# Kernel tuning notes

Hardware: AMD Instinct MI355X
Metric: run time of the kernel (lower is better)

## Reference

```python
import jax, jax.numpy as jnp
import numpy as np

N_NODES = 50000
N_EDGES = 800000
IN_FEAT = 128
HEADS = 4
UNITS = 16
LEAKY_ALPHA = 0.2  # tf.nn.leaky_relu default


def setup_inputs() -> dict:
    key = jax.random.key(0)
    k1, k2, k3, k4, k5 = jax.random.split(key, 5)
    x = jax.random.normal(k1, (N_NODES, IN_FEAT), dtype=jnp.float32)
    edge_index = jax.random.randint(k2, (N_EDGES, 2), 0, N_NODES, dtype=jnp.int32)
    # Dense kernel (glorot-ish scaling), no bias (use_bias=False)
    W = jax.random.normal(k3, (IN_FEAT, HEADS * UNITS), dtype=jnp.float32) * (1.0 / np.sqrt(IN_FEAT))
    glorot = np.sqrt(2.0 / (1 + UNITS)).astype(np.float32)
    att_w1 = jax.random.normal(k4, (HEADS, 1, UNITS), dtype=jnp.float32) * glorot
    att_w2 = jax.random.normal(k5, (HEADS, 1, UNITS), dtype=jnp.float32) * glorot
    return {"x": x, "edge_index": edge_index, "W": W, "att_w1": att_w1, "att_w2": att_w2}


def reference(x, edge_index, W, att_w1, att_w2):
    n_nodes = x.shape[0]
    h = x @ W  # [N, H*U]
    snd_idx = edge_index[:, 0]
    rcv_idx = edge_index[:, 1]
    # gather per-edge features, split into heads -> [H, E, U]
    sender = h[snd_idx].reshape(-1, HEADS, UNITS).transpose(1, 0, 2)
    receiver = h[rcv_idx].reshape(-1, HEADS, UNITS).transpose(1, 0, 2)
    # per-edge, per-head attention logits [H, E]
    att = jnp.sum(att_w1 * sender, axis=-1) + jnp.sum(att_w2 * receiver, axis=-1)
    att = jnp.where(att > 0, att, LEAKY_ALPHA * att)
    # segment softmax over receiver neighborhoods, per head
    seg_max = jax.vmap(lambda a: jax.ops.segment_max(a, rcv_idx, num_segments=n_nodes))(att)  # [H, N]
    e = jnp.exp(att - seg_max[:, rcv_idx])
    denom = jax.vmap(lambda a: jax.ops.segment_sum(a, rcv_idx, num_segments=n_nodes))(e)  # [H, N]
    alpha = e / denom[:, rcv_idx]  # [H, E]
    # weighted scatter-sum of sender features -> [H, N, U]
    out = jax.vmap(lambda v: jax.ops.segment_sum(v, rcv_idx, num_segments=n_nodes))(sender * alpha[:, :, None])
    # concat heads -> [N, H*U]; activation is None (identity)
    return out.transpose(1, 0, 2).reshape(n_nodes, HEADS * UNITS)
```

## Files before the change

### kernel.cpp

```cpp
#include <hip/hip_runtime.h>
#include <math.h>

#define N_NODES 50000
#define N_EDGES 800000
#define IN_FEAT 128
#define HEADS   4
#define UNITS   16
#define OUTF    64
#define LEAKY   0.2f

#define NB      196
#define BCAP    5120
#define GEMM_BLKS 782
#define A_BLOCKS  391
#define EPB     8

typedef __attribute__((ext_vector_type(8))) short bf16x8;
typedef __attribute__((ext_vector_type(4))) float f32x4;

__device__ __forceinline__ unsigned short f2bf(float f) {
    unsigned u = __float_as_uint(f);
    unsigned r = u + 0x7FFFu + ((u >> 16) & 1u);
    return (unsigned short)(r >> 16);
}

union SharedU {
    struct { unsigned short xl[64 * 136]; unsigned short wt[64 * 136]; } g;
    struct { int2 stage[2048]; int hist[256], s[256], excl[256],
             gbase[256], cur[256]; } a;
};

__global__ __launch_bounds__(256) void wt_prep(const float* __restrict__ W,
                                               unsigned short* __restrict__ Wt_g,
                                               int* __restrict__ bucket_cnt) {
    int idx = blockIdx.x * 256 + threadIdx.x;
    if (blockIdx.x == 0 && threadIdx.x < NB) bucket_cnt[threadIdx.x] = 0;
    if (idx < IN_FEAT * OUTF) {
        int k = idx >> 6, c = idx & 63;
        Wt_g[c * IN_FEAT + k] = f2bf(W[idx]);
    }
}

__global__ __launch_bounds__(256) void fused_gemm_bucketA(const float* __restrict__ x,
                                                          const unsigned short* __restrict__ Wt_g,
                                                          const float* __restrict__ w1,
                                                          const float* __restrict__ w2,
                                                          const int2* __restrict__ ei,
                                                          unsigned short* __restrict__ hg,
                                                          float* __restrict__ a1,
                                                          float* __restrict__ a2,
                                                          int* __restrict__ bucket_cnt,
                                                          int2* __restrict__ buckets) {
    __shared__ SharedU sh;
    const int t = threadIdx.x;

    if (blockIdx.x >= GEMM_BLKS) {
        const int e0 = (blockIdx.x - GEMM_BLKS) * 2048;
        sh.a.hist[t] = 0;
        __syncthreads();

        int2 ed[EPB]; int bk[EPB];
        #pragma unroll
        for (int j = 0; j < EPB; ++j) {
            int e = e0 + t + j * 256;
            if (e < N_EDGES) {
                ed[j] = ei[e];
                bk[j] = ed[j].y >> 8;
                atomicAdd(&sh.a.hist[bk[j]], 1);
            } else bk[j] = -1;
        }
        __syncthreads();
        int v = sh.a.hist[t];
        sh.a.s[t] = v;
        __syncthreads();
        #pragma unroll
        for (int off = 1; off < 256; off <<= 1) {
            int u = (t >= off) ? sh.a.s[t - off] : 0;
            __syncthreads();
            sh.a.s[t] += u;
            __syncthreads();
        }
        sh.a.excl[t] = sh.a.s[t] - v;
        sh.a.cur[t] = 0;
        if (t < NB) sh.a.gbase[t] = atomicAdd(&bucket_cnt[t], v);
        __syncthreads();
        #pragma unroll
        for (int j = 0; j < EPB; ++j) {
            if (bk[j] >= 0) {
                int p = sh.a.excl[bk[j]] + atomicAdd(&sh.a.cur[bk[j]], 1);
                sh.a.stage[p] = ed[j];
            }
        }
        __syncthreads();
        const int total = min(2048, N_EDGES - e0);
        for (int i = t; i < total; i += 256) {
            int2 vv = sh.a.stage[i];
            int b = vv.y >> 8;
            buckets[(size_t)b * BCAP + sh.a.gbase[b] + (i - sh.a.excl[b])] = vv;
        }
        return;
    }

    const int node0 = blockIdx.x * 64;
    unsigned short* xl = sh.g.xl;
    unsigned short* wt = sh.g.wt;

    #pragma unroll
    for (int it = 0; it < 8; ++it) {
        int idx = t + 256 * it;
        int r = idx >> 5, q = idx & 31;
        int node = node0 + r;
        float4 v = make_float4(0.f, 0.f, 0.f, 0.f);
        if (node < N_NODES) v = *(const float4*)(x + (size_t)node * IN_FEAT + q * 4);
        ushort4 b;
        b.x = f2bf(v.x); b.y = f2bf(v.y); b.z = f2bf(v.z); b.w = f2bf(v.w);
        *(ushort4*)&xl[r * 136 + q * 4] = b;
    }
    {
        const ushort4* Wt4 = (const ushort4*)Wt_g;
        #pragma unroll
        for (int it = 0; it < 8; ++it) {
            int idx = t + 256 * it;
            int c = idx >> 5, u = idx & 31;
            *(ushort4*)&wt[c * 136 + u * 4] = Wt4[idx];
        }
    }
    __syncthreads();

    const int lane = t & 63, wv = t >> 6;
    const int m = lane & 15, quad = lane >> 4;
    const int n0 = wv * 16;

    f32x4 acc[4] = {{0,0,0,0},{0,0,0,0},{0,0,0,0},{0,0,0,0}};
    #pragma unroll
    for (int kc = 0; kc < 4; ++kc) {
        bf16x8 af = *(bf16x8*)&xl[(n0 + m) * 136 + kc * 32 + quad * 8];
        #pragma unroll
        for (int ct = 0; ct < 4; ++ct) {
            bf16x8 bfr = *(bf16x8*)&wt[(ct * 16 + m) * 136 + kc * 32 + quad * 8];
            acc[ct] = __builtin_amdgcn_mfma_f32_16x16x32_bf16(af, bfr, acc[ct], 0, 0, 0);
        }
    }

    #pragma unroll
    for (int ct = 0; ct < 4; ++ct) {
        const float u1 = w1[ct * 16 + m];
        const float u2 = w2[ct * 16 + m];
        #pragma unroll
        for (int r = 0; r < 4; ++r) {
            float p1 = acc[ct][r] * u1;
            float p2 = acc[ct][r] * u2;
            p1 += __shfl_xor(p1, 1, 64); p1 += __shfl_xor(p1, 2, 64);
            p1 += __shfl_xor(p1, 4, 64); p1 += __shfl_xor(p1, 8, 64);
            p2 += __shfl_xor(p2, 1, 64); p2 += __shfl_xor(p2, 2, 64);
            p2 += __shfl_xor(p2, 4, 64); p2 += __shfl_xor(p2, 8, 64);
            if (m == 0) {
                int node = node0 + n0 + quad * 4 + r;
                if (node < N_NODES) {
                    a1[node * 4 + ct] = p1;
                    a2[node * 4 + ct] = p2;
                }
            }
        }
    }

    __syncthreads();
    unsigned short* hl = sh.g.xl;
    #pragma unroll
    for (int ct = 0; ct < 4; ++ct)
        #pragma unroll
        for (int r = 0; r < 4; ++r)
            hl[(n0 + quad * 4 + r) * 72 + ct * 16 + m] = f2bf(acc[ct][r]);
    __syncthreads();
    #pragma unroll
    for (int it = 0; it < 2; ++it) {
        int u = t + 256 * it;
        int r = u >> 3, cg = u & 7;
        int node = node0 + r;
        if (node < N_NODES)
            *(uint4*)&hg[(size_t)node * OUTF + cg * 8] = *(uint4*)&hl[r * 72 + cg * 8];
    }
}

__global__ __launch_bounds__(256) void bucketB(const int2* __restrict__ buckets,
                                               const int* __restrict__ bucket_cnt,
                                               int* __restrict__ edge_snd,
                                               int* __restrict__ rs,
                                               int* __restrict__ re) {
    __shared__ int hist[256], cur[256], s[256];
    __shared__ int snds[BCAP];
    const int b = blockIdx.x;
    const int t = threadIdx.x;
    const int cnt = bucket_cnt[b];
    hist[t] = 0;
    __syncthreads();
    for (int i = t; i < cnt; i += 256)
        atomicAdd(&hist[buckets[(size_t)b * BCAP + i].y & 255], 1);
    __syncthreads();
    int v = hist[t];
    s[t] = v;
    __syncthreads();
    #pragma unroll
    for (int off = 1; off < 256; off <<= 1) {
        int u = (t >= off) ? s[t - off] : 0;
        __syncthreads();
        s[t] += u;
        __syncthreads();
    }
    const int excl = s[t] - v;
    cur[t] = excl;
    const int node = b * 256 + t;
    if (node < N_NODES) {
        rs[node] = b * BCAP + excl;
        re[node] = b * BCAP + excl + v;
    }
    __syncthreads();
    for (int i = t; i < cnt; i += 256) {
        int2 vv = buckets[(size_t)b * BCAP + i];
        int p = atomicAdd(&cur[vv.y & 255], 1);
        snds[p] = vv.x;
    }
    __syncthreads();
    for (int i = t; i < cnt; i += 256) edge_snd[(size_t)b * BCAP + i] = snds[i];
}

__global__ __launch_bounds__(256, 8) void gather_kernel(const int* __restrict__ rs,
                                                        const int* __restrict__ re,
                                                        const int* __restrict__ edge_snd,
                                                        const float* __restrict__ a1,
                                                        const float* __restrict__ a2,
                                                        const unsigned short* __restrict__ h,
                                                        float* __restrict__ out) {
    const int wave = threadIdx.x >> 6;
    const int lane = threadIdx.x & 63;
    const int n = blockIdx.x * 4 + wave;
    if (n >= N_NODES) return;
    const int sub  = lane >> 3;
    const int li   = lane & 7;
    const int head = li >> 1;
    const int base = rs[n];
    const int end  = re[n];
    if (end <= base) {
        if (sub == 0) {
            *(float4*)(out + (size_t)n * OUTF + li * 8)     = make_float4(0.f, 0.f, 0.f, 0.f);
            *(float4*)(out + (size_t)n * OUTF + li * 8 + 4) = make_float4(0.f, 0.f, 0.f, 0.f);
        }
        return;
    }
    const float a2h = a2[n * 4 + head];
    const uint4* h4 = (const uint4*)h;

    float acc[8] = {0.f,0.f,0.f,0.f,0.f,0.f,0.f,0.f};
    float den = 0.f;

    for (int i = base; i < end; i += 16) {
        #pragma unroll
        for (int g = 0; g < 2; ++g) {
            int eraw = i + g * 8 + sub;
            int eidx = min(eraw, end - 1);
            int s = edge_snd[eidx];
            float t0 = a1[s * 4 + head] + a2h;
            t0 = t0 > 0.f ? t0 : LEAKY * t0;
            float e = (eraw < end) ? __expf(t0) : 0.f;
            uint4 hv = h4[(unsigned)(s * 8 + li)];
            const unsigned hw[4] = {hv.x, hv.y, hv.z, hv.w};
            #pragma unroll
            for (int q = 0; q < 4; ++q) {
                acc[q*2+0] = fmaf(e, __uint_as_float(hw[q] << 16),         acc[q*2+0]);
                acc[q*2+1] = fmaf(e, __uint_as_float(hw[q] & 0xFFFF0000u), acc[q*2+1]);
            }
            den += e;
        }
    }

    #pragma unroll
    for (int off = 8; off <= 32; off <<= 1) {
        #pragma unroll
        for (int q = 0; q < 8; ++q) acc[q] += __shfl_xor(acc[q], off, 64);
        den += __shfl_xor(den, off, 64);
    }

    if (sub == 0) {
        float inv = 1.f / den;
        *(float4*)(out + (size_t)n * OUTF + li * 8) =
            make_float4(acc[0] * inv, acc[1] * inv, acc[2] * inv, acc[3] * inv);
        *(float4*)(out + (size_t)n * OUTF + li * 8 + 4) =
            make_float4(acc[4] * inv, acc[5] * inv, acc[6] * inv, acc[7] * inv);
    }
}

extern "C" void kernel_launch(void* const* d_in, const int* in_sizes, int n_in,
                              void* d_out, int out_size, void* d_ws, size_t ws_size,
                              hipStream_t stream) {
    const float* x  = (const float*)d_in[0];
    const int2*  ei = (const int2*)d_in[1];
    const float* W  = (const float*)d_in[2];
    const float* w1 = (const float*)d_in[3];
    const float* w2 = (const float*)d_in[4];
    float* out = (float*)d_out;

    unsigned short* h = (unsigned short*)d_ws;
    float* a1         = (float*)(h + (size_t)N_NODES * OUTF);
    float* a2         = a1 + (size_t)N_NODES * HEADS;
    int2*  buckets    = (int2*)(a2 + (size_t)N_NODES * HEADS);
    int*   edge_snd   = (int*)(buckets + (size_t)NB * BCAP);
    int*   rs         = edge_snd + (size_t)NB * BCAP;
    int*   re         = rs + N_NODES;
    int*   bucket_cnt = re + N_NODES;
    unsigned short* Wt_g = (unsigned short*)(bucket_cnt + NB);

    wt_prep<<<32, 256, 0, stream>>>(W, Wt_g, bucket_cnt);
    fused_gemm_bucketA<<<GEMM_BLKS + A_BLOCKS, 256, 0, stream>>>(x, Wt_g, w1, w2, ei,
                                                                 h, a1, a2,
                                                                 bucket_cnt, buckets);
    bucketB<<<NB, 256, 0, stream>>>(buckets, bucket_cnt, edge_snd, rs, re);
    gather_kernel<<<(N_NODES + 3) / 4, 256, 0, stream>>>(rs, re, edge_snd, a1, a2, h, out);
}
```

Measured before the change: 134.8 us.

## Precompute per-edge attention exponentials in bucketB and fold W transpose into GEMM

Removes the wt_prep kernel: every GEMM block now converts and transposes W from fp32 itself, and bucket_cnt is cleared with a memset. bucketB is widened to 1024 threads, stages the bucket in shared memory to avoid reading it twice, and computes all four heads' leaky-relu exponentials per edge, writing them to a new edge_e array. The gather kernel then reads the precomputed e values instead of doing a random a1 lookup and an exp. The cost is an extra 16 bytes per edge written and read, plus a scattered 2-byte shared-memory transpose store of W in every GEMM block.

```diff
diff --git a/kernel.cpp b/kernel.cpp
--- a/kernel.cpp
+++ b/kernel.cpp
@@ -30,19 +30,8 @@
              gbase[256], cur[256]; } a;
 };
 
-__global__ __launch_bounds__(256) void wt_prep(const float* __restrict__ W,
-                                               unsigned short* __restrict__ Wt_g,
-                                               int* __restrict__ bucket_cnt) {
-    int idx = blockIdx.x * 256 + threadIdx.x;
-    if (blockIdx.x == 0 && threadIdx.x < NB) bucket_cnt[threadIdx.x] = 0;
-    if (idx < IN_FEAT * OUTF) {
-        int k = idx >> 6, c = idx & 63;
-        Wt_g[c * IN_FEAT + k] = f2bf(W[idx]);
-    }
-}
-
 __global__ __launch_bounds__(256) void fused_gemm_bucketA(const float* __restrict__ x,
-                                                          const unsigned short* __restrict__ Wt_g,
+                                                          const float* __restrict__ W,
                                                           const float* __restrict__ w1,
                                                           const float* __restrict__ w2,
                                                           const int2* __restrict__ ei,
@@ -117,12 +106,17 @@
         *(ushort4*)&xl[r * 136 + q * 4] = b;
     }
     {
-        const ushort4* Wt4 = (const ushort4*)Wt_g;
+        const float4* W4 = (const float4*)W;
         #pragma unroll
         for (int it = 0; it < 8; ++it) {
-            int idx = t + 256 * it;
-            int c = idx >> 5, u = idx & 31;
-            *(ushort4*)&wt[c * 136 + u * 4] = Wt4[idx];
+            int idx4 = t + 256 * it;
+            float4 v = W4[idx4];
+            int flat = idx4 * 4;
+            int k = flat >> 6, c = flat & 63;
+            wt[(c + 0) * 136 + k] = f2bf(v.x);
+            wt[(c + 1) * 136 + k] = f2bf(v.y);
+            wt[(c + 2) * 136 + k] = f2bf(v.z);
+            wt[(c + 3) * 136 + k] = f2bf(v.w);
         }
     }
     __syncthreads();
@@ -182,53 +176,67 @@
     }
 }
 
-__global__ __launch_bounds__(256) void bucketB(const int2* __restrict__ buckets,
-                                               const int* __restrict__ bucket_cnt,
-                                               int* __restrict__ edge_snd,
-                                               int* __restrict__ rs,
-                                               int* __restrict__ re) {
+__global__ __launch_bounds__(1024) void bucketB(const int2* __restrict__ buckets,
+                                                const int* __restrict__ bucket_cnt,
+                                                const float* __restrict__ a1,
+                                                const float* __restrict__ a2,
+                                                int* __restrict__ edge_snd,
+                                                float* __restrict__ edge_e,
+                                                int* __restrict__ rs,
+                                                int* __restrict__ re) {
     __shared__ int hist[256], cur[256], s[256];
-    __shared__ int snds[BCAP];
+    __shared__ int2 stage[BCAP];
     const int b = blockIdx.x;
     const int t = threadIdx.x;
     const int cnt = bucket_cnt[b];
-    hist[t] = 0;
-    __syncthreads();
-    for (int i = t; i < cnt; i += 256)
-        atomicAdd(&hist[buckets[(size_t)b * BCAP + i].y & 255], 1);
-    __syncthreads();
-    int v = hist[t];
-    s[t] = v;
+    if (t < 256) hist[t] = 0;
+    __syncthreads();
+    for (int i = t; i < cnt; i += 1024) {
+        int2 vv = buckets[(size_t)b * BCAP + i];
+        stage[i] = vv;
+        atomicAdd(&hist[vv.y & 255], 1);
+    }
+    __syncthreads();
+    if (t < 256) s[t] = hist[t];
     __syncthreads();
     #pragma unroll
     for (int off = 1; off < 256; off <<= 1) {
-        int u = (t >= off) ? s[t - off] : 0;
-        __syncthreads();
-        s[t] += u;
-        __syncthreads();
-    }
-    const int excl = s[t] - v;
-    cur[t] = excl;
-    const int node = b * 256 + t;
-    if (node < N_NODES) {
-        rs[node] = b * BCAP + excl;
-        re[node] = b * BCAP + excl + v;
-    }
-    __syncthreads();
-    for (int i = t; i < cnt; i += 256) {
-        int2 vv = buckets[(size_t)b * BCAP + i];
+        int u = (t < 256 && t >= off) ? s[t - off] : 0;
+        __syncthreads();
+        if (t < 256) s[t] += u;
+        __syncthreads();
+    }
+    if (t < 256) {
+        const int v = hist[t];
+        const int excl = s[t] - v;
+        cur[t] = excl;
+        const int node = b * 256 + t;
+        if (node < N_NODES) {
+            rs[node] = b * BCAP + excl;
+            re[node] = b * BCAP + excl + v;
+        }
+    }
+    __syncthreads();
+    for (int i = t; i < cnt; i += 1024) {
+        int2 vv = stage[i];
         int p = atomicAdd(&cur[vv.y & 255], 1);
-        snds[p] = vv.x;
-    }
-    __syncthreads();
-    for (int i = t; i < cnt; i += 256) edge_snd[(size_t)b * BCAP + i] = snds[i];
+        float4 s1 = *(const float4*)(a1 + (size_t)vv.x * 4);
+        float4 s2 = *(const float4*)(a2 + (size_t)vv.y * 4);
+        float t0 = s1.x + s2.x; t0 = t0 > 0.f ? t0 : LEAKY * t0;
+        float t1 = s1.y + s2.y; t1 = t1 > 0.f ? t1 : LEAKY * t1;
+        float t2 = s1.z + s2.z; t2 = t2 > 0.f ? t2 : LEAKY * t2;
+        float t3 = s1.w + s2.w; t3 = t3 > 0.f ? t3 : LEAKY * t3;
+        float4 e4 = make_float4(__expf(t0), __expf(t1), __expf(t2), __expf(t3));
+        size_t q = (size_t)b * BCAP + p;
+        edge_snd[q] = vv.x;
+        *(float4*)(edge_e + q * 4) = e4;
+    }
 }
 
 __global__ __launch_bounds__(256, 8) void gather_kernel(const int* __restrict__ rs,
                                                         const int* __restrict__ re,
                                                         const int* __restrict__ edge_snd,
-                                                        const float* __restrict__ a1,
-                                                        const float* __restrict__ a2,
+                                                        const float* __restrict__ edge_e,
                                                         const unsigned short* __restrict__ h,
                                                         float* __restrict__ out) {
     const int wave = threadIdx.x >> 6;
@@ -247,7 +255,6 @@
         }
         return;
     }
-    const float a2h = a2[n * 4 + head];
     const uint4* h4 = (const uint4*)h;
 
     float acc[8] = {0.f,0.f,0.f,0.f,0.f,0.f,0.f,0.f};
@@ -259,9 +266,8 @@
             int eraw = i + g * 8 + sub;
             int eidx = min(eraw, end - 1);
             int s = edge_snd[eidx];
-            float t0 = a1[s * 4 + head] + a2h;
-            t0 = t0 > 0.f ? t0 : LEAKY * t0;
-            float e = (eraw < end) ? __expf(t0) : 0.f;
+            float ev = edge_e[(size_t)eidx * 4 + head];
+            float e = (eraw < end) ? ev : 0.f;
             uint4 hv = h4[(unsigned)(s * 8 + li)];
             const unsigned hw[4] = {hv.x, hv.y, hv.z, hv.w};
             #pragma unroll
@@ -303,16 +309,17 @@
     float* a1         = (float*)(h + (size_t)N_NODES * OUTF);
     float* a2         = a1 + (size_t)N_NODES * HEADS;
     int2*  buckets    = (int2*)(a2 + (size_t)N_NODES * HEADS);
-    int*   edge_snd   = (int*)(buckets + (size_t)NB * BCAP);
+    float* edge_e     = (float*)(buckets + (size_t)NB * BCAP);
+    int*   edge_snd   = (int*)(edge_e + (size_t)NB * BCAP * 4);
     int*   rs         = edge_snd + (size_t)NB * BCAP;
     int*   re         = rs + N_NODES;
     int*   bucket_cnt = re + N_NODES;
-    unsigned short* Wt_g = (unsigned short*)(bucket_cnt + NB);
-
-    wt_prep<<<32, 256, 0, stream>>>(W, Wt_g, bucket_cnt);
-    fused_gemm_bucketA<<<GEMM_BLKS + A_BLOCKS, 256, 0, stream>>>(x, Wt_g, w1, w2, ei,
+
+    hipMemsetAsync(bucket_cnt, 0, NB * sizeof(int), stream);
+    fused_gemm_bucketA<<<GEMM_BLKS + A_BLOCKS, 256, 0, stream>>>(x, W, w1, w2, ei,
                                                                  h, a1, a2,
                                                                  bucket_cnt, buckets);
-    bucketB<<<NB, 256, 0, stream>>>(buckets, bucket_cnt, edge_snd, rs, re);
-    gather_kernel<<<(N_NODES + 3) / 4, 256, 0, stream>>>(rs, re, edge_snd, a1, a2, h, out);
-}
+    bucketB<<<NB, 1024, 0, stream>>>(buckets, bucket_cnt, a1, a2,
+                                     edge_snd, edge_e, rs, re);
+    gather_kernel<<<(N_NODES + 3) / 4, 256, 0, stream>>>(rs, re, edge_snd, edge_e, h, out);
+}
```

New measurement: 136.5 us. Within noise of the previous version (+1.3%).

## Fold attention vectors into weights, use wave-shuffle scans, widen bucketB blocks

Applied to the files above, without the earlier changes.

Precomputes W·att_w1 and W·att_w2 per head in the prep kernel, split into bf16 hi/lo parts, so the attention logits come from one extra MFMA per k-chunk instead of a shuffle-reduction epilogue. Replaces the shared-memory Hillis-Steele scans in both bucketing kernels with wave-level shuffle scans plus cross-wave offsets, and simplifies the global scatter offset. bucketB now runs 1024 threads, stages edges in LDS to avoid reading them twice, and writes sender ids directly to global, dropping the final copy loop. Extra LDS in the GEMM path and the launch_bounds occupancy hint may change occupancy, and the bf16 hi/lo split slightly changes logit precision.

```diff
diff --git a/kernel.cpp b/kernel.cpp
--- a/kernel.cpp
+++ b/kernel.cpp
@@ -23,36 +23,58 @@
     unsigned r = u + 0x7FFFu + ((u >> 16) & 1u);
     return (unsigned short)(r >> 16);
 }
+__device__ __forceinline__ float bf2f(unsigned short b) {
+    return __uint_as_float(((unsigned)b) << 16);
+}
 
 union SharedU {
-    struct { unsigned short xl[64 * 136]; unsigned short wt[64 * 136]; } g;
-    struct { int2 stage[2048]; int hist[256], s[256], excl[256],
-             gbase[256], cur[256]; } a;
+    struct { unsigned short xl[64 * 136]; unsigned short wt[64 * 136];
+             unsigned short wa[16 * 136]; } g;
+    struct { int2 stage[2048]; int hist[256], cur[256], adj[256], wsum[4]; } a;
 };
 
-__global__ __launch_bounds__(256) void wt_prep(const float* __restrict__ W,
-                                               unsigned short* __restrict__ Wt_g,
-                                               int* __restrict__ bucket_cnt) {
+__global__ __launch_bounds__(256) void prep(const float* __restrict__ W,
+                                            const float* __restrict__ w1,
+                                            const float* __restrict__ w2,
+                                            unsigned short* __restrict__ Wt_g,
+                                            unsigned short* __restrict__ Wea_g,
+                                            int* __restrict__ bucket_cnt) {
     int idx = blockIdx.x * 256 + threadIdx.x;
-    if (blockIdx.x == 0 && threadIdx.x < NB) bucket_cnt[threadIdx.x] = 0;
+    if (idx < NB) bucket_cnt[idx] = 0;
     if (idx < IN_FEAT * OUTF) {
         int k = idx >> 6, c = idx & 63;
         Wt_g[c * IN_FEAT + k] = f2bf(W[idx]);
     }
-}
-
-__global__ __launch_bounds__(256) void fused_gemm_bucketA(const float* __restrict__ x,
-                                                          const unsigned short* __restrict__ Wt_g,
-                                                          const float* __restrict__ w1,
-                                                          const float* __restrict__ w2,
-                                                          const int2* __restrict__ ei,
-                                                          unsigned short* __restrict__ hg,
-                                                          float* __restrict__ a1,
-                                                          float* __restrict__ a2,
-                                                          int* __restrict__ bucket_cnt,
-                                                          int2* __restrict__ buckets) {
+    if (idx < IN_FEAT * HEADS) {
+        int k = idx >> 2, hd = idx & 3;
+        float s1 = 0.f, s2 = 0.f;
+        #pragma unroll
+        for (int u = 0; u < UNITS; ++u) {
+            float wv = W[k * OUTF + hd * UNITS + u];
+            s1 += wv * w1[hd * UNITS + u];
+            s2 += wv * w2[hd * UNITS + u];
+        }
+        unsigned short h1 = f2bf(s1), h2 = f2bf(s2);
+        unsigned short l1 = f2bf(s1 - bf2f(h1)), l2 = f2bf(s2 - bf2f(h2));
+        Wea_g[(hd)      * IN_FEAT + k] = h1;
+        Wea_g[(4 + hd)  * IN_FEAT + k] = h2;
+        Wea_g[(8 + hd)  * IN_FEAT + k] = l1;
+        Wea_g[(12 + hd) * IN_FEAT + k] = l2;
+    }
+}
+
+__global__ __launch_bounds__(256, 4) void fused_gemm_bucketA(const float* __restrict__ x,
+                                                             const unsigned short* __restrict__ Wt_g,
+                                                             const unsigned short* __restrict__ Wea_g,
+                                                             const int2* __restrict__ ei,
+                                                             unsigned short* __restrict__ hg,
+                                                             float* __restrict__ a1,
+                                                             float* __restrict__ a2,
+                                                             int* __restrict__ bucket_cnt,
+                                                             int2* __restrict__ buckets) {
     __shared__ SharedU sh;
     const int t = threadIdx.x;
+    const int lane = t & 63, wv = t >> 6;
 
     if (blockIdx.x >= GEMM_BLKS) {
         const int e0 = (blockIdx.x - GEMM_BLKS) * 2048;
@@ -70,24 +92,28 @@
             } else bk[j] = -1;
         }
         __syncthreads();
-        int v = sh.a.hist[t];
-        sh.a.s[t] = v;
-        __syncthreads();
-        #pragma unroll
-        for (int off = 1; off < 256; off <<= 1) {
-            int u = (t >= off) ? sh.a.s[t - off] : 0;
-            __syncthreads();
-            sh.a.s[t] += u;
-            __syncthreads();
-        }
-        sh.a.excl[t] = sh.a.s[t] - v;
-        sh.a.cur[t] = 0;
-        if (t < NB) sh.a.gbase[t] = atomicAdd(&bucket_cnt[t], v);
+        const int v = sh.a.hist[t];
+        int inc = v;
+        #pragma unroll
+        for (int off = 1; off < 64; off <<= 1) {
+            int u = __shfl_up(inc, off, 64);
+            if (lane >= off) inc += u;
+        }
+        if (lane == 63) sh.a.wsum[wv] = inc;
+        __syncthreads();
+        const int s0 = sh.a.wsum[0], s1 = sh.a.wsum[1], s2 = sh.a.wsum[2];
+        const int wo = (wv > 0 ? s0 : 0) + (wv > 1 ? s1 : 0) + (wv > 2 ? s2 : 0);
+        const int excl = wo + inc - v;
+        sh.a.cur[t] = excl;
+        if (t < NB) {
+            int g0 = atomicAdd(&bucket_cnt[t], v);
+            sh.a.adj[t] = g0 - excl;
+        }
         __syncthreads();
         #pragma unroll
         for (int j = 0; j < EPB; ++j) {
             if (bk[j] >= 0) {
-                int p = sh.a.excl[bk[j]] + atomicAdd(&sh.a.cur[bk[j]], 1);
+                int p = atomicAdd(&sh.a.cur[bk[j]], 1);
                 sh.a.stage[p] = ed[j];
             }
         }
@@ -96,7 +122,7 @@
         for (int i = t; i < total; i += 256) {
             int2 vv = sh.a.stage[i];
             int b = vv.y >> 8;
-            buckets[(size_t)b * BCAP + sh.a.gbase[b] + (i - sh.a.excl[b])] = vv;
+            buckets[(size_t)(b * BCAP + sh.a.adj[b] + i)] = vv;
         }
         return;
     }
@@ -104,6 +130,7 @@
     const int node0 = blockIdx.x * 64;
     unsigned short* xl = sh.g.xl;
     unsigned short* wt = sh.g.wt;
+    unsigned short* wa = sh.g.wa;
 
     #pragma unroll
     for (int it = 0; it < 8; ++it) {
@@ -124,14 +151,21 @@
             int c = idx >> 5, u = idx & 31;
             *(ushort4*)&wt[c * 136 + u * 4] = Wt4[idx];
         }
-    }
-    __syncthreads();
-
-    const int lane = t & 63, wv = t >> 6;
+        const ushort4* Wa4 = (const ushort4*)Wea_g;
+        {
+            int idx = t, c = idx >> 5, u = idx & 31;
+            *(ushort4*)&wa[c * 136 + u * 4] = Wa4[idx];
+            idx = t + 256; c = idx >> 5; u = idx & 31;
+            *(ushort4*)&wa[c * 136 + u * 4] = Wa4[idx];
+        }
+    }
+    __syncthreads();
+
     const int m = lane & 15, quad = lane >> 4;
     const int n0 = wv * 16;
 
     f32x4 acc[4] = {{0,0,0,0},{0,0,0,0},{0,0,0,0},{0,0,0,0}};
+    f32x4 acca   = {0,0,0,0};
     #pragma unroll
     for (int kc = 0; kc < 4; ++kc) {
         bf16x8 af = *(bf16x8*)&xl[(n0 + m) * 136 + kc * 32 + quad * 8];
@@ -140,27 +174,17 @@
             bf16x8 bfr = *(bf16x8*)&wt[(ct * 16 + m) * 136 + kc * 32 + quad * 8];
             acc[ct] = __builtin_amdgcn_mfma_f32_16x16x32_bf16(af, bfr, acc[ct], 0, 0, 0);
         }
-    }
-
-    #pragma unroll
-    for (int ct = 0; ct < 4; ++ct) {
-        const float u1 = w1[ct * 16 + m];
-        const float u2 = w2[ct * 16 + m];
-        #pragma unroll
-        for (int r = 0; r < 4; ++r) {
-            float p1 = acc[ct][r] * u1;
-            float p2 = acc[ct][r] * u2;
-            p1 += __shfl_xor(p1, 1, 64); p1 += __shfl_xor(p1, 2, 64);
-            p1 += __shfl_xor(p1, 4, 64); p1 += __shfl_xor(p1, 8, 64);
-            p2 += __shfl_xor(p2, 1, 64); p2 += __shfl_xor(p2, 2, 64);
-            p2 += __shfl_xor(p2, 4, 64); p2 += __shfl_xor(p2, 8, 64);
-            if (m == 0) {
-                int node = node0 + n0 + quad * 4 + r;
-                if (node < N_NODES) {
-                    a1[node * 4 + ct] = p1;
-                    a2[node * 4 + ct] = p2;
-                }
-            }
+        bf16x8 waf = *(bf16x8*)&wa[m * 136 + kc * 32 + quad * 8];
+        acca = __builtin_amdgcn_mfma_f32_16x16x32_bf16(af, waf, acca, 0, 0, 0);
+    }
+
+    #pragma unroll
+    for (int r = 0; r < 4; ++r) {
+        float vres = acca[r] + __shfl_xor(acca[r], 8, 64);
+        int node = node0 + n0 + quad * 4 + r;
+        if (node < N_NODES) {
+            if (m < 4)      a1[node * 4 + m]       = vres;
+            else if (m < 8) a2[node * 4 + (m - 4)] = vres;
         }
     }
 
@@ -182,46 +206,55 @@
     }
 }
 
-__global__ __launch_bounds__(256) void bucketB(const int2* __restrict__ buckets,
-                                               const int* __restrict__ bucket_cnt,
-                                               int* __restrict__ edge_snd,
-                                               int* __restrict__ rs,
-                                               int* __restrict__ re) {
-    __shared__ int hist[256], cur[256], s[256];
-    __shared__ int snds[BCAP];
+__global__ __launch_bounds__(1024) void bucketB(const int2* __restrict__ buckets,
+                                                const int* __restrict__ bucket_cnt,
+                                                int* __restrict__ edge_snd,
+                                                int* __restrict__ rs,
+                                                int* __restrict__ re) {
+    __shared__ int2 stage[BCAP];
+    __shared__ int hist[256], cur[256], wsum[4];
     const int b = blockIdx.x;
     const int t = threadIdx.x;
     const int cnt = bucket_cnt[b];
-    hist[t] = 0;
-    __syncthreads();
-    for (int i = t; i < cnt; i += 256)
-        atomicAdd(&hist[buckets[(size_t)b * BCAP + i].y & 255], 1);
-    __syncthreads();
-    int v = hist[t];
-    s[t] = v;
-    __syncthreads();
-    #pragma unroll
-    for (int off = 1; off < 256; off <<= 1) {
-        int u = (t >= off) ? s[t - off] : 0;
-        __syncthreads();
-        s[t] += u;
-        __syncthreads();
-    }
-    const int excl = s[t] - v;
-    cur[t] = excl;
-    const int node = b * 256 + t;
-    if (node < N_NODES) {
-        rs[node] = b * BCAP + excl;
-        re[node] = b * BCAP + excl + v;
-    }
-    __syncthreads();
-    for (int i = t; i < cnt; i += 256) {
+    if (t < 256) hist[t] = 0;
+    __syncthreads();
+    for (int i = t; i < cnt; i += 1024) {
         int2 vv = buckets[(size_t)b * BCAP + i];
+        stage[i] = vv;
+        atomicAdd(&hist[vv.y & 255], 1);
+    }
+    __syncthreads();
+    int v = 0, inc = 0;
+    if (t < 256) {
+        const int lane = t & 63, wvx = t >> 6;
+        v = hist[t];
+        inc = v;
+        #pragma unroll
+        for (int off = 1; off < 64; off <<= 1) {
+            int u = __shfl_up(inc, off, 64);
+            if (lane >= off) inc += u;
+        }
+        if (lane == 63) wsum[wvx] = inc;
+    }
+    __syncthreads();
+    if (t < 256) {
+        const int wvx = t >> 6;
+        const int s0 = wsum[0], s1 = wsum[1], s2 = wsum[2];
+        const int wo = (wvx > 0 ? s0 : 0) + (wvx > 1 ? s1 : 0) + (wvx > 2 ? s2 : 0);
+        const int excl = wo + inc - v;
+        cur[t] = excl;
+        const int node = b * 256 + t;
+        if (node < N_NODES) {
+            rs[node] = b * BCAP + excl;
+            re[node] = b * BCAP + excl + v;
+        }
+    }
+    __syncthreads();
+    for (int i = t; i < cnt; i += 1024) {
+        int2 vv = stage[i];
         int p = atomicAdd(&cur[vv.y & 255], 1);
-        snds[p] = vv.x;
-    }
-    __syncthreads();
-    for (int i = t; i < cnt; i += 256) edge_snd[(size_t)b * BCAP + i] = snds[i];
+        edge_snd[(size_t)b * BCAP + p] = vv.x;
+    }
 }
 
 __global__ __launch_bounds__(256, 8) void gather_kernel(const int* __restrict__ rs,
@@ -299,20 +332,21 @@
     const float* w2 = (const float*)d_in[4];
     float* out = (float*)d_out;
 
-    unsigned short* h = (unsigned short*)d_ws;
-    float* a1         = (float*)(h + (size_t)N_NODES * OUTF);
-    float* a2         = a1 + (size_t)N_NODES * HEADS;
-    int2*  buckets    = (int2*)(a2 + (size_t)N_NODES * HEADS);
-    int*   edge_snd   = (int*)(buckets + (size_t)NB * BCAP);
-    int*   rs         = edge_snd + (size_t)NB * BCAP;
-    int*   re         = rs + N_NODES;
-    int*   bucket_cnt = re + N_NODES;
-    unsigned short* Wt_g = (unsigned short*)(bucket_cnt + NB);
-
-    wt_prep<<<32, 256, 0, stream>>>(W, Wt_g, bucket_cnt);
-    fused_gemm_bucketA<<<GEMM_BLKS + A_BLOCKS, 256, 0, stream>>>(x, Wt_g, w1, w2, ei,
+    unsigned short* h    = (unsigned short*)d_ws;
+    float* a1            = (float*)(h + (size_t)N_NODES * OUTF);
+    float* a2            = a1 + (size_t)N_NODES * HEADS;
+    unsigned short* Wt_g = (unsigned short*)(a2 + (size_t)N_NODES * HEADS);
+    unsigned short* Wea_g = Wt_g + IN_FEAT * OUTF;
+    int*   bucket_cnt    = (int*)(Wea_g + IN_FEAT * 16);
+    int2*  buckets       = (int2*)(bucket_cnt + 256);
+    int*   edge_snd      = (int*)(buckets + (size_t)NB * BCAP);
+    int*   rs            = edge_snd + (size_t)NB * BCAP;
+    int*   re            = rs + N_NODES;
+
+    prep<<<32, 256, 0, stream>>>(W, w1, w2, Wt_g, Wea_g, bucket_cnt);
+    fused_gemm_bucketA<<<GEMM_BLKS + A_BLOCKS, 256, 0, stream>>>(x, Wt_g, Wea_g, ei,
                                                                  h, a1, a2,
                                                                  bucket_cnt, buckets);
-    bucketB<<<NB, 256, 0, stream>>>(buckets, bucket_cnt, edge_snd, rs, re);
+    bucketB<<<NB, 1024, 0, stream>>>(buckets, bucket_cnt, edge_snd, rs, re);
     gather_kernel<<<(N_NODES + 3) / 4, 256, 0, stream>>>(rs, re, edge_snd, a1, a2, h, out);
 }
```

Result: faster. 130.0 us (-3.5%).
